# Kernel tuning notes

Measured on AMD Instinct MI355X. Metric: run time of the kernel, lower is better.

## Reference

```python
import jax, jax.numpy as jnp
import numpy as np


def setup_inputs() -> dict:
    key = jax.random.key(0)
    k1, k2, k3, k4 = jax.random.split(key, 4)
    T, H, E, I = 4096, 1024, 8, 3584
    return {
        "hidden_states": jax.random.normal(k1, (T, H), dtype=jnp.float32),
        "gate_w": jax.random.normal(k2, (H, E), dtype=jnp.float32) * 0.02,
        "w1": jax.random.normal(k3, (E, H, I), dtype=jnp.float32) * 0.02,
        "w2": jax.random.normal(k4, (E, I, H), dtype=jnp.float32) * 0.02,
        "top_k": 2,
    }


def reference(hidden_states, gate_w, w1, w2, top_k):
    # Router: logits -> softmax -> top-k -> renormalize (Mixtral / vLLM fused_moe)
    router_logits = hidden_states @ gate_w                    # [T, E]
    probs = jax.nn.softmax(router_logits, axis=-1)
    top_vals, top_idx = jax.lax.top_k(probs, top_k)           # [T, K]
    top_vals = top_vals / jnp.sum(top_vals, axis=-1, keepdims=True)
    E = gate_w.shape[1]
    # Dense per-(token, expert) combine weights, zero for non-selected experts
    dense_w = jnp.sum(jax.nn.one_hot(top_idx, E, dtype=hidden_states.dtype)
                      * top_vals[..., None], axis=1)          # [T, E]
    # Expert MLP: silu(x @ w1[e]) @ w2[e], weighted by routing probs
    act = jax.nn.silu(jnp.einsum('th,ehi->tei', hidden_states, w1))  # [T, E, I]
    act = act * dense_w[:, :, None]
    out = jnp.einsum('tei,eih->th', act, w2)                  # [T, H]
    return out
```

## Files before the change

### kernel.cpp

```cpp
#include <hip/hip_runtime.h>
#include <hip/hip_bf16.h>

#define T_TOK 4096
#define H_DIM 1024
#define E_NUM 8
#define I_DIM 3584
#define NPAIR (T_TOK * 2)
#define MAX_RT 72

#define BM 128
#define BN 128
#define BK 64

typedef __attribute__((ext_vector_type(8))) short bf16x8;
typedef __attribute__((ext_vector_type(4))) float f32x4;
typedef __attribute__((ext_vector_type(8))) unsigned short ushort8_t;
typedef __attribute__((ext_vector_type(4))) unsigned short ushort4_t;

__device__ __forceinline__ unsigned short f2bf(float x) {
  unsigned int u = __float_as_uint(x);
  unsigned int r = (u + 0x7FFFu + ((u >> 16) & 1u)) >> 16;
  return (unsigned short)r;
}

__device__ __forceinline__ void gload16(const void* g, unsigned short* l) {
  __builtin_amdgcn_global_load_lds(
      (const __attribute__((address_space(1))) void*)g,
      (__attribute__((address_space(3))) void*)l, 16, 0, 0);
}

__global__ void transpose_cvt(const float* __restrict__ src,
                              unsigned short* __restrict__ dst, int R, int C) {
  __shared__ float tile[64][65];
  const int e = blockIdx.z;
  const int c0 = blockIdx.x * 64, r0 = blockIdx.y * 64;
  const float* s = src + (size_t)e * R * C;
  unsigned short* d = dst + (size_t)e * R * C;
  const int th = threadIdx.x;
  const int tr = th >> 4;
  const int tc4 = (th & 15) * 4;
#pragma unroll
  for (int it = 0; it < 4; ++it) {
    const int r = it * 16 + tr;
    float4 v = *reinterpret_cast<const float4*>(s + (size_t)(r0 + r) * C + c0 + tc4);
    tile[r][tc4] = v.x; tile[r][tc4 + 1] = v.y; tile[r][tc4 + 2] = v.z; tile[r][tc4 + 3] = v.w;
  }
  __syncthreads();
  const int wc = th >> 3;
  const int wr = (th & 7) * 8;
#pragma unroll
  for (int it = 0; it < 2; ++it) {
    const int c = it * 32 + wc;
    ushort8_t o;
#pragma unroll
    for (int j = 0; j < 8; ++j) o[j] = f2bf(tile[wr + j][c]);
    *reinterpret_cast<ushort8_t*>(d + (size_t)(c0 + c) * R + r0 + wr) = o;
  }
}

__global__ void router_kernel(const float* __restrict__ hs, const float* __restrict__ gw,
                              unsigned short* __restrict__ hsb,
                              int* __restrict__ eid, float* __restrict__ wgt,
                              int* __restrict__ counts) {
  __shared__ float s_gw[8192];
  __shared__ int s_cnt[E_NUM];
  const int th = threadIdx.x;
  for (int u = th; u < 2048; u += 256) {
    const f32x4 v = *reinterpret_cast<const f32x4*>(gw + u * 4);
    *reinterpret_cast<f32x4*>(&s_gw[(u ^ ((u >> 3) & 7)) * 4]) = v;
  }
  if (th < E_NUM) s_cnt[th] = 0;
  __syncthreads();

  const int l = th & 63, w = th >> 6;
#pragma unroll 1
  for (int tt = 0; tt < 4; ++tt) {
    const int t = blockIdx.x * 16 + w * 4 + tt;
    const float* hrow = hs + (size_t)t * H_DIM;
    unsigned short* brow = hsb + (size_t)t * H_DIM;
    float acc[E_NUM];
#pragma unroll
    for (int e = 0; e < E_NUM; ++e) acc[e] = 0.f;
#pragma unroll
    for (int i = 0; i < 4; ++i) {
      const int h0 = i * 256 + l * 4;
      const f32x4 x = *reinterpret_cast<const f32x4*>(hrow + h0);
      ushort4_t o = { f2bf(x[0]), f2bf(x[1]), f2bf(x[2]), f2bf(x[3]) };
      *reinterpret_cast<ushort4_t*>(brow + h0) = o;
#pragma unroll
      for (int j = 0; j < 4; ++j) {
        const int h = h0 + j;
        const int p0 = (h * 2) ^ ((h >> 2) & 7);
        const f32x4 g0 = *reinterpret_cast<const f32x4*>(&s_gw[p0 * 4]);
        const f32x4 g1 = *reinterpret_cast<const f32x4*>(&s_gw[(p0 ^ 1) * 4]);
        acc[0] += x[j] * g0[0]; acc[1] += x[j] * g0[1];
        acc[2] += x[j] * g0[2]; acc[3] += x[j] * g0[3];
        acc[4] += x[j] * g1[0]; acc[5] += x[j] * g1[1];
        acc[6] += x[j] * g1[2]; acc[7] += x[j] * g1[3];
      }
    }
#pragma unroll
    for (int e = 0; e < E_NUM; ++e) {
#pragma unroll
      for (int off = 1; off < 64; off <<= 1) acc[e] += __shfl_xor(acc[e], off);
    }
    if (l == 0) {
      int i1 = 0;
#pragma unroll
      for (int e = 1; e < E_NUM; ++e) if (acc[e] > acc[i1]) i1 = e;
      int i2 = (i1 == 0) ? 1 : 0;
#pragma unroll
      for (int e = 0; e < E_NUM; ++e) if (e != i1 && acc[e] > acc[i2]) i2 = e;
      const float e2 = __expf(acc[i2] - acc[i1]);
      const float inv = 1.f / (1.f + e2);
      eid[t * 2] = i1;     wgt[t * 2] = inv;
      eid[t * 2 + 1] = i2; wgt[t * 2 + 1] = e2 * inv;
      atomicAdd(&s_cnt[i1], 1);
      atomicAdd(&s_cnt[i2], 1);
    }
  }
  __syncthreads();
  if (th < E_NUM && s_cnt[th] > 0) atomicAdd(&counts[th], s_cnt[th]);
}

__global__ void scatter_kernel(const int* __restrict__ eid, const int* __restrict__ counts,
                               int* __restrict__ fill, int* __restrict__ rowmap,
                               int* __restrict__ posmap) {
  __shared__ int hist[E_NUM], base[E_NUM];
  const int th = threadIdx.x;
  const int p = blockIdx.x * 256 + th;
  if (th < E_NUM) hist[th] = 0;
  __syncthreads();
  const int e = eid[p];
  const int rloc = atomicAdd(&hist[e], 1);
  __syncthreads();
  if (th < E_NUM) base[th] = (hist[th] > 0) ? atomicAdd(&fill[th], hist[th]) : 0;
  __syncthreads();
  int off = 0;
#pragma unroll
  for (int i = 0; i < E_NUM; ++i) off += (i < e) ? counts[i] : 0;
  const int pos = off + base[e] + rloc;
  rowmap[pos] = p;
  posmap[p] = pos;
}

__global__ void combine_kernel(const float* __restrict__ res, const int* __restrict__ posmap,
                               float* __restrict__ out) {
  const int t = blockIdx.x;
  const int th = threadIdx.x;
  const int a = posmap[t * 2];
  const int b = posmap[t * 2 + 1];
  const float4 va = *reinterpret_cast<const float4*>(res + (size_t)a * H_DIM + th * 4);
  const float4 vb = *reinterpret_cast<const float4*>(res + (size_t)b * H_DIM + th * 4);
  float4 o = { va.x + vb.x, va.y + vb.y, va.z + vb.z, va.w + vb.w };
  *reinterpret_cast<float4*>(out + (size_t)t * H_DIM + th * 4) = o;
}

template <int MODE, int NCT>
__launch_bounds__(256, 4)
__global__ void moe_gemm(const unsigned short* __restrict__ hsb,
                         const unsigned short* __restrict__ wt,
                         const unsigned short* __restrict__ act_in,
                         unsigned short* __restrict__ act_out,
                         float* __restrict__ res,
                         const int* __restrict__ counts,
                         const int* __restrict__ rowmap,
                         const float* __restrict__ wgt) {
  constexpr int KD = (MODE == 0) ? H_DIM : I_DIM;
  constexpr int NWG = MAX_RT * NCT;

  __shared__ unsigned short As[BM * BK];
  __shared__ unsigned short Bs[BN * BK];
  __shared__ float s_w[BM];

  const int bid = blockIdx.x;
  const int wgid = (bid & 7) * (NWG / 8) + (bid >> 3);
  const int rt = wgid / NCT;
  const int ct = wgid % NCT;

  int e = -1, loc_rt = 0, off_e = 0, cnt = 0;
  {
    int acc_t = 0, off = 0;
#pragma unroll
    for (int ee = 0; ee < E_NUM; ++ee) {
      const int c = counts[ee];
      const int nt = (c + BM - 1) >> 7;
      if (e < 0 && rt < acc_t + nt) { e = ee; loc_rt = rt - acc_t; off_e = off; cnt = c; }
      acc_t += nt; off += c;
    }
  }
  if (e < 0) return;

  const int cnt_local = min(BM, cnt - loc_rt * BM);
  const int r_base = off_e + loc_rt * BM;
  const int th = threadIdx.x;
  const int lane = th & 63, wid = th >> 6;

  if (MODE == 1 && th < BM) {
    int r = loc_rt * BM + th;
    if (r >= cnt) r = cnt - 1;
    s_w[th] = wgt[rowmap[off_e + r]];
  }

  const int n0 = ct * BN;
  const unsigned short* wbase = wt + (size_t)e * ((size_t)I_DIM * H_DIM) + (size_t)n0 * KD;

  const int srow = lane >> 3;
  const int cg = (lane & 7) ^ srow;
  const char* aptr[4];
  const char* bptr[4];
#pragma unroll
  for (int i = 0; i < 4; ++i) {
    const int r = i * 32 + wid * 8 + srow;
    const int rr = (r < cnt_local) ? r : (cnt_local - 1);
    if (MODE == 0) {
      const int tok = rowmap[off_e + loc_rt * BM + rr] >> 1;
      aptr[i] = (const char*)(hsb + (size_t)tok * H_DIM) + cg * 16;
    } else {
      aptr[i] = (const char*)(act_in + (size_t)(r_base + rr) * I_DIM) + cg * 16;
    }
    bptr[i] = (const char*)(wbase + (size_t)r * KD) + cg * 16;
  }
  unsigned short* dstA[4];
  unsigned short* dstB[4];
#pragma unroll
  for (int i = 0; i < 4; ++i) {
    dstA[i] = &As[(i * 32 + wid * 8) * BK];
    dstB[i] = &Bs[(i * 32 + wid * 8) * BK];
  }

  f32x4 acc[4][4];
#pragma unroll
  for (int m = 0; m < 4; ++m)
#pragma unroll
    for (int n = 0; n < 4; ++n) acc[m][n] = (f32x4){0.f, 0.f, 0.f, 0.f};

  const int wm = (wid >> 1) * 64;
  const int wn = (wid & 1) * 64;
  const int fr = lane & 15;
  const int fq = lane >> 4;
  const int sxor = fr & 7;

  for (int k0 = 0; k0 < KD; k0 += BK) {
    const int kb = k0 * 2;
#pragma unroll
    for (int i = 0; i < 4; ++i) gload16(aptr[i] + kb, dstA[i]);
#pragma unroll
    for (int i = 0; i < 4; ++i) gload16(bptr[i] + kb, dstB[i]);
    __syncthreads();

#pragma unroll
    for (int kk = 0; kk < 2; ++kk) {
      bf16x8 af[4], bf[4];
#pragma unroll
      for (int m = 0; m < 4; ++m)
        af[m] = *reinterpret_cast<const bf16x8*>(
            &As[(wm + m * 16 + fr) * BK + ((kk * 4 + fq) ^ sxor) * 8]);
#pragma unroll
      for (int n = 0; n < 4; ++n)
        bf[n] = *reinterpret_cast<const bf16x8*>(
            &Bs[(wn + n * 16 + fr) * BK + ((kk * 4 + fq) ^ sxor) * 8]);
#pragma unroll
      for (int m = 0; m < 4; ++m)
#pragma unroll
        for (int n = 0; n < 4; ++n)
          acc[m][n] = __builtin_amdgcn_mfma_f32_16x16x32_bf16(af[m], bf[n], acc[m][n], 0, 0, 0);
    }
    __syncthreads();
  }

#pragma unroll
  for (int m = 0; m < 4; ++m) {
    const int row = wm + m * 16 + fq * 4;
#pragma unroll
    for (int n = 0; n < 4; ++n) {
      const int col = wn + n * 16 + fr;
#pragma unroll
      for (int r = 0; r < 4; ++r) {
        const int rw = row + r;
        if (rw < cnt_local) {
          const float x = acc[m][n][r];
          if (MODE == 0) {
            const float s = x / (1.f + __expf(-x));
            act_out[(size_t)(r_base + rw) * I_DIM + n0 + col] = f2bf(s);
          } else {
            res[(size_t)(r_base + rw) * H_DIM + n0 + col] = x * s_w[rw];
          }
        }
      }
    }
  }
}

extern "C" void kernel_launch(void* const* d_in, const int* in_sizes, int n_in,
                              void* d_out, int out_size, void* d_ws, size_t ws_size,
                              hipStream_t stream) {
  const float* hs = (const float*)d_in[0];
  const float* gw = (const float*)d_in[1];
  const float* w1 = (const float*)d_in[2];
  const float* w2 = (const float*)d_in[3];
  float* out = (float*)d_out;

  char* ws = (char*)d_ws;
  const size_t WMAT = (size_t)E_NUM * I_DIM * H_DIM * 2;
  unsigned short* w1t = (unsigned short*)ws;
  unsigned short* w2t = (unsigned short*)(ws + WMAT);
  unsigned short* act = (unsigned short*)(ws + 2 * WMAT);
  unsigned short* hsb = (unsigned short*)(ws + 3 * WMAT);
  float* res = (float*)w1t;
  char* small = ws + 3 * WMAT + (size_t)T_TOK * H_DIM * 2;
  int* eid = (int*)small;
  float* wgt = (float*)(small + NPAIR * 4);
  int* rowmap = (int*)(small + 2 * NPAIR * 4);
  int* posmap = (int*)(small + 3 * NPAIR * 4);
  int* counts = (int*)(small + 4 * NPAIR * 4);
  int* fill = counts + 8;

  hipMemsetAsync(counts, 0, 16 * sizeof(int), stream);

  transpose_cvt<<<dim3(I_DIM / 64, H_DIM / 64, E_NUM), 256, 0, stream>>>(w1, w1t, H_DIM, I_DIM);
  transpose_cvt<<<dim3(H_DIM / 64, I_DIM / 64, E_NUM), 256, 0, stream>>>(w2, w2t, I_DIM, H_DIM);

  router_kernel<<<T_TOK / 16, 256, 0, stream>>>(hs, gw, hsb, eid, wgt, counts);
  scatter_kernel<<<NPAIR / 256, 256, 0, stream>>>(eid, counts, fill, rowmap, posmap);

  moe_gemm<0, I_DIM / BN><<<MAX_RT * (I_DIM / BN), 256, 0, stream>>>(
      hsb, w1t, nullptr, act, nullptr, counts, rowmap, wgt);
  moe_gemm<1, H_DIM / BN><<<MAX_RT * (H_DIM / BN), 256, 0, stream>>>(
      hsb, w2t, act, nullptr, res, counts, rowmap, wgt);

  combine_kernel<<<T_TOK, 256, 0, stream>>>(res, posmap, out);
}
```

Baseline: 286.3 us.

## Fuse weight transposes and router into one prep kernel; narrow second GEMM tile

Merges the two weight transpose-convert launches and the router launch into a single prep kernel that picks its role by block index and shares one shared-memory buffer. This removes two launches and lets the router work overlap with the tail of the transposes. The down-projection GEMM drops to a 64-wide N tile with a 4x1 warp layout and an occupancy hint of 5. That doubles its workgroup count, giving better CU fill on the small N dimension, at the cost of less reuse of the A tile.

```diff
diff --git a/kernel.cpp b/kernel.cpp
--- a/kernel.cpp
+++ b/kernel.cpp
@@ -9,7 +9,6 @@
 #define MAX_RT 72
 
 #define BM 128
-#define BN 128
 #define BK 64
 
 typedef __attribute__((ext_vector_type(8))) short bf16x8;
@@ -29,11 +28,11 @@
       (__attribute__((address_space(3))) void*)l, 16, 0, 0);
 }
 
-__global__ void transpose_cvt(const float* __restrict__ src,
-                              unsigned short* __restrict__ dst, int R, int C) {
-  __shared__ float tile[64][65];
-  const int e = blockIdx.z;
-  const int c0 = blockIdx.x * 64, r0 = blockIdx.y * 64;
+__device__ __forceinline__ void transpose_body(const float* __restrict__ src,
+                                               unsigned short* __restrict__ dst,
+                                               int R, int C, int e, int c0, int r0,
+                                               char* smem) {
+  float (*tile)[65] = reinterpret_cast<float (*)[65]>(smem);
   const float* s = src + (size_t)e * R * C;
   unsigned short* d = dst + (size_t)e * R * C;
   const int th = threadIdx.x;
@@ -58,12 +57,13 @@
   }
 }
 
-__global__ void router_kernel(const float* __restrict__ hs, const float* __restrict__ gw,
-                              unsigned short* __restrict__ hsb,
-                              int* __restrict__ eid, float* __restrict__ wgt,
-                              int* __restrict__ counts) {
-  __shared__ float s_gw[8192];
-  __shared__ int s_cnt[E_NUM];
+__device__ __forceinline__ void router_body(const float* __restrict__ hs,
+                                            const float* __restrict__ gw,
+                                            unsigned short* __restrict__ hsb,
+                                            int* __restrict__ eid, float* __restrict__ wgt,
+                                            int* __restrict__ counts, int rbid, char* smem) {
+  float* s_gw = reinterpret_cast<float*>(smem);
+  int* s_cnt = reinterpret_cast<int*>(smem + 32768);
   const int th = threadIdx.x;
   for (int u = th; u < 2048; u += 256) {
     const f32x4 v = *reinterpret_cast<const f32x4*>(gw + u * 4);
@@ -75,7 +75,7 @@
   const int l = th & 63, w = th >> 6;
 #pragma unroll 1
   for (int tt = 0; tt < 4; ++tt) {
-    const int t = blockIdx.x * 16 + w * 4 + tt;
+    const int t = rbid * 16 + w * 4 + tt;
     const float* hrow = hs + (size_t)t * H_DIM;
     unsigned short* brow = hsb + (size_t)t * H_DIM;
     float acc[E_NUM];
@@ -123,6 +123,26 @@
   if (th < E_NUM && s_cnt[th] > 0) atomicAdd(&counts[th], s_cnt[th]);
 }
 
+__global__ __launch_bounds__(256) void prep_kernel(
+    const float* __restrict__ w1, const float* __restrict__ w2,
+    const float* __restrict__ hs, const float* __restrict__ gw,
+    unsigned short* __restrict__ w1t, unsigned short* __restrict__ w2t,
+    unsigned short* __restrict__ hsb,
+    int* __restrict__ eid, float* __restrict__ wgt, int* __restrict__ counts) {
+  __shared__ char smem[33024];
+  const int bid = blockIdx.x;
+  if (bid < 7168) {
+    const int e = bid / 896, rem = bid % 896;
+    transpose_body(w1, w1t, H_DIM, I_DIM, e, (rem % 56) * 64, (rem / 56) * 64, smem);
+  } else if (bid < 14336) {
+    const int idx = bid - 7168;
+    const int e = idx / 896, rem = idx % 896;
+    transpose_body(w2, w2t, I_DIM, H_DIM, e, (rem % 16) * 64, (rem / 16) * 64, smem);
+  } else {
+    router_body(hs, gw, hsb, eid, wgt, counts, bid - 14336, smem);
+  }
+}
+
 __global__ void scatter_kernel(const int* __restrict__ eid, const int* __restrict__ counts,
                                int* __restrict__ fill, int* __restrict__ rowmap,
                                int* __restrict__ posmap) {
@@ -156,8 +176,8 @@
   *reinterpret_cast<float4*>(out + (size_t)t * H_DIM + th * 4) = o;
 }
 
-template <int MODE, int NCT>
-__launch_bounds__(256, 4)
+template <int MODE, int NCT, int OCC>
+__launch_bounds__(256, OCC)
 __global__ void moe_gemm(const unsigned short* __restrict__ hsb,
                          const unsigned short* __restrict__ wt,
                          const unsigned short* __restrict__ act_in,
@@ -167,10 +187,13 @@
                          const int* __restrict__ rowmap,
                          const float* __restrict__ wgt) {
   constexpr int KD = (MODE == 0) ? H_DIM : I_DIM;
+  constexpr int BN_ = (MODE == 0) ? 128 : 64;
+  constexpr int MFR = (MODE == 0) ? 4 : 2;
+  constexpr int NBR = BN_ / 32;
   constexpr int NWG = MAX_RT * NCT;
 
   __shared__ unsigned short As[BM * BK];
-  __shared__ unsigned short Bs[BN * BK];
+  __shared__ unsigned short Bs[BN_ * BK];
   __shared__ float s_w[BM];
 
   const int bid = blockIdx.x;
@@ -202,13 +225,13 @@
     s_w[th] = wgt[rowmap[off_e + r]];
   }
 
-  const int n0 = ct * BN;
+  const int n0 = ct * BN_;
   const unsigned short* wbase = wt + (size_t)e * ((size_t)I_DIM * H_DIM) + (size_t)n0 * KD;
 
   const int srow = lane >> 3;
   const int cg = (lane & 7) ^ srow;
   const char* aptr[4];
-  const char* bptr[4];
+  const char* bptr[NBR];
 #pragma unroll
   for (int i = 0; i < 4; ++i) {
     const int r = i * 32 + wid * 8 + srow;
@@ -219,24 +242,27 @@
     } else {
       aptr[i] = (const char*)(act_in + (size_t)(r_base + rr) * I_DIM) + cg * 16;
     }
-    bptr[i] = (const char*)(wbase + (size_t)r * KD) + cg * 16;
+  }
+#pragma unroll
+  for (int j = 0; j < NBR; ++j) {
+    const int r = j * 32 + wid * 8 + srow;
+    bptr[j] = (const char*)(wbase + (size_t)r * KD) + cg * 16;
   }
   unsigned short* dstA[4];
-  unsigned short* dstB[4];
-#pragma unroll
-  for (int i = 0; i < 4; ++i) {
-    dstA[i] = &As[(i * 32 + wid * 8) * BK];
-    dstB[i] = &Bs[(i * 32 + wid * 8) * BK];
-  }
-
-  f32x4 acc[4][4];
-#pragma unroll
-  for (int m = 0; m < 4; ++m)
+  unsigned short* dstB[NBR];
+#pragma unroll
+  for (int i = 0; i < 4; ++i) dstA[i] = &As[(i * 32 + wid * 8) * BK];
+#pragma unroll
+  for (int j = 0; j < NBR; ++j) dstB[j] = &Bs[(j * 32 + wid * 8) * BK];
+
+  f32x4 acc[MFR][4];
+#pragma unroll
+  for (int m = 0; m < MFR; ++m)
 #pragma unroll
     for (int n = 0; n < 4; ++n) acc[m][n] = (f32x4){0.f, 0.f, 0.f, 0.f};
 
-  const int wm = (wid >> 1) * 64;
-  const int wn = (wid & 1) * 64;
+  const int wm = (MODE == 0) ? (wid >> 1) * 64 : wid * 32;
+  const int wn = (MODE == 0) ? (wid & 1) * 64 : 0;
   const int fr = lane & 15;
   const int fq = lane >> 4;
   const int sxor = fr & 7;
@@ -246,14 +272,14 @@
 #pragma unroll
     for (int i = 0; i < 4; ++i) gload16(aptr[i] + kb, dstA[i]);
 #pragma unroll
-    for (int i = 0; i < 4; ++i) gload16(bptr[i] + kb, dstB[i]);
+    for (int j = 0; j < NBR; ++j) gload16(bptr[j] + kb, dstB[j]);
     __syncthreads();
 
 #pragma unroll
     for (int kk = 0; kk < 2; ++kk) {
-      bf16x8 af[4], bf[4];
-#pragma unroll
-      for (int m = 0; m < 4; ++m)
+      bf16x8 af[MFR], bf[4];
+#pragma unroll
+      for (int m = 0; m < MFR; ++m)
         af[m] = *reinterpret_cast<const bf16x8*>(
             &As[(wm + m * 16 + fr) * BK + ((kk * 4 + fq) ^ sxor) * 8]);
 #pragma unroll
@@ -261,7 +287,7 @@
         bf[n] = *reinterpret_cast<const bf16x8*>(
             &Bs[(wn + n * 16 + fr) * BK + ((kk * 4 + fq) ^ sxor) * 8]);
 #pragma unroll
-      for (int m = 0; m < 4; ++m)
+      for (int m = 0; m < MFR; ++m)
 #pragma unroll
         for (int n = 0; n < 4; ++n)
           acc[m][n] = __builtin_amdgcn_mfma_f32_16x16x32_bf16(af[m], bf[n], acc[m][n], 0, 0, 0);
@@ -270,7 +296,7 @@
   }
 
 #pragma unroll
-  for (int m = 0; m < 4; ++m) {
+  for (int m = 0; m < MFR; ++m) {
     const int row = wm + m * 16 + fq * 4;
 #pragma unroll
     for (int n = 0; n < 4; ++n) {
@@ -318,15 +344,12 @@
 
   hipMemsetAsync(counts, 0, 16 * sizeof(int), stream);
 
-  transpose_cvt<<<dim3(I_DIM / 64, H_DIM / 64, E_NUM), 256, 0, stream>>>(w1, w1t, H_DIM, I_DIM);
-  transpose_cvt<<<dim3(H_DIM / 64, I_DIM / 64, E_NUM), 256, 0, stream>>>(w2, w2t, I_DIM, H_DIM);
-
-  router_kernel<<<T_TOK / 16, 256, 0, stream>>>(hs, gw, hsb, eid, wgt, counts);
+  prep_kernel<<<14592, 256, 0, stream>>>(w1, w2, hs, gw, w1t, w2t, hsb, eid, wgt, counts);
   scatter_kernel<<<NPAIR / 256, 256, 0, stream>>>(eid, counts, fill, rowmap, posmap);
 
-  moe_gemm<0, I_DIM / BN><<<MAX_RT * (I_DIM / BN), 256, 0, stream>>>(
+  moe_gemm<0, I_DIM / 128, 4><<<MAX_RT * (I_DIM / 128), 256, 0, stream>>>(
       hsb, w1t, nullptr, act, nullptr, counts, rowmap, wgt);
-  moe_gemm<1, H_DIM / BN><<<MAX_RT * (H_DIM / BN), 256, 0, stream>>>(
+  moe_gemm<1, H_DIM / 64, 5><<<MAX_RT * (H_DIM / 64), 256, 0, stream>>>(
       hsb, w2t, act, nullptr, res, counts, rowmap, wgt);
 
   combine_kernel<<<T_TOK, 256, 0, stream>>>(res, posmap, out);
```

Result: faster. 261.1 us (-8.8%).

## Shrink GEMM N-tile to 64, raise occupancy, and merge weight transposes into one launch

Applied to the files above, without the earlier changes.

Halves the GEMM tile width (BN 128→64), reorganizing the four waves as a 4x1 stack of 32-row slices that each hold half as many accumulators. The minimum-blocks hint in launch bounds goes from 4 to 5 for more occupancy and twice as many workgroups. The two weight transpose-convert launches are merged into one launch with a flat block index. The trade-off is lower arithmetic intensity per tile, so A tiles are reloaded twice as often.

```diff
diff --git a/kernel.cpp b/kernel.cpp
--- a/kernel.cpp
+++ b/kernel.cpp
@@ -9,7 +9,7 @@
 #define MAX_RT 72
 
 #define BM 128
-#define BN 128
+#define BN 64
 #define BK 64
 
 typedef __attribute__((ext_vector_type(8))) short bf16x8;
@@ -29,11 +29,25 @@
       (__attribute__((address_space(3))) void*)l, 16, 0, 0);
 }
 
-__global__ void transpose_cvt(const float* __restrict__ src,
-                              unsigned short* __restrict__ dst, int R, int C) {
+__global__ __launch_bounds__(256) void wt_transpose(
+    const float* __restrict__ w1, const float* __restrict__ w2,
+    unsigned short* __restrict__ w1t, unsigned short* __restrict__ w2t) {
   __shared__ float tile[64][65];
-  const int e = blockIdx.z;
-  const int c0 = blockIdx.x * 64, r0 = blockIdx.y * 64;
+  const int bid = blockIdx.x;
+  const float* src;
+  unsigned short* dst;
+  int R, C, e, c0, r0;
+  if (bid < 7168) {
+    const int rem = bid % 896;
+    e = bid / 896; R = H_DIM; C = I_DIM;
+    c0 = (rem % 56) * 64; r0 = (rem / 56) * 64;
+    src = w1; dst = w1t;
+  } else {
+    const int idx = bid - 7168, rem = idx % 896;
+    e = idx / 896; R = I_DIM; C = H_DIM;
+    c0 = (rem % 16) * 64; r0 = (rem / 16) * 64;
+    src = w2; dst = w2t;
+  }
   const float* s = src + (size_t)e * R * C;
   unsigned short* d = dst + (size_t)e * R * C;
   const int th = threadIdx.x;
@@ -157,7 +171,7 @@
 }
 
 template <int MODE, int NCT>
-__launch_bounds__(256, 4)
+__launch_bounds__(256, 5)
 __global__ void moe_gemm(const unsigned short* __restrict__ hsb,
                          const unsigned short* __restrict__ wt,
                          const unsigned short* __restrict__ act_in,
@@ -208,7 +222,7 @@
   const int srow = lane >> 3;
   const int cg = (lane & 7) ^ srow;
   const char* aptr[4];
-  const char* bptr[4];
+  const char* bptr[2];
 #pragma unroll
   for (int i = 0; i < 4; ++i) {
     const int r = i * 32 + wid * 8 + srow;
@@ -219,24 +233,26 @@
     } else {
       aptr[i] = (const char*)(act_in + (size_t)(r_base + rr) * I_DIM) + cg * 16;
     }
-    bptr[i] = (const char*)(wbase + (size_t)r * KD) + cg * 16;
+  }
+#pragma unroll
+  for (int j = 0; j < 2; ++j) {
+    const int r = j * 32 + wid * 8 + srow;
+    bptr[j] = (const char*)(wbase + (size_t)r * KD) + cg * 16;
   }
   unsigned short* dstA[4];
-  unsigned short* dstB[4];
-#pragma unroll
-  for (int i = 0; i < 4; ++i) {
-    dstA[i] = &As[(i * 32 + wid * 8) * BK];
-    dstB[i] = &Bs[(i * 32 + wid * 8) * BK];
-  }
-
-  f32x4 acc[4][4];
-#pragma unroll
-  for (int m = 0; m < 4; ++m)
+  unsigned short* dstB[2];
+#pragma unroll
+  for (int i = 0; i < 4; ++i) dstA[i] = &As[(i * 32 + wid * 8) * BK];
+#pragma unroll
+  for (int j = 0; j < 2; ++j) dstB[j] = &Bs[(j * 32 + wid * 8) * BK];
+
+  f32x4 acc[2][4];
+#pragma unroll
+  for (int m = 0; m < 2; ++m)
 #pragma unroll
     for (int n = 0; n < 4; ++n) acc[m][n] = (f32x4){0.f, 0.f, 0.f, 0.f};
 
-  const int wm = (wid >> 1) * 64;
-  const int wn = (wid & 1) * 64;
+  const int wm = wid * 32;
   const int fr = lane & 15;
   const int fq = lane >> 4;
   const int sxor = fr & 7;
@@ -246,22 +262,22 @@
 #pragma unroll
     for (int i = 0; i < 4; ++i) gload16(aptr[i] + kb, dstA[i]);
 #pragma unroll
-    for (int i = 0; i < 4; ++i) gload16(bptr[i] + kb, dstB[i]);
+    for (int j = 0; j < 2; ++j) gload16(bptr[j] + kb, dstB[j]);
     __syncthreads();
 
 #pragma unroll
     for (int kk = 0; kk < 2; ++kk) {
-      bf16x8 af[4], bf[4];
-#pragma unroll
-      for (int m = 0; m < 4; ++m)
+      bf16x8 af[2], bf[4];
+#pragma unroll
+      for (int m = 0; m < 2; ++m)
         af[m] = *reinterpret_cast<const bf16x8*>(
             &As[(wm + m * 16 + fr) * BK + ((kk * 4 + fq) ^ sxor) * 8]);
 #pragma unroll
       for (int n = 0; n < 4; ++n)
         bf[n] = *reinterpret_cast<const bf16x8*>(
-            &Bs[(wn + n * 16 + fr) * BK + ((kk * 4 + fq) ^ sxor) * 8]);
-#pragma unroll
-      for (int m = 0; m < 4; ++m)
+            &Bs[(n * 16 + fr) * BK + ((kk * 4 + fq) ^ sxor) * 8]);
+#pragma unroll
+      for (int m = 0; m < 2; ++m)
 #pragma unroll
         for (int n = 0; n < 4; ++n)
           acc[m][n] = __builtin_amdgcn_mfma_f32_16x16x32_bf16(af[m], bf[n], acc[m][n], 0, 0, 0);
@@ -270,11 +286,11 @@
   }
 
 #pragma unroll
-  for (int m = 0; m < 4; ++m) {
+  for (int m = 0; m < 2; ++m) {
     const int row = wm + m * 16 + fq * 4;
 #pragma unroll
     for (int n = 0; n < 4; ++n) {
-      const int col = wn + n * 16 + fr;
+      const int col = n0 + n * 16 + fr;
 #pragma unroll
       for (int r = 0; r < 4; ++r) {
         const int rw = row + r;
@@ -282,9 +298,9 @@
           const float x = acc[m][n][r];
           if (MODE == 0) {
             const float s = x / (1.f + __expf(-x));
-            act_out[(size_t)(r_base + rw) * I_DIM + n0 + col] = f2bf(s);
+            act_out[(size_t)(r_base + rw) * I_DIM + col] = f2bf(s);
           } else {
-            res[(size_t)(r_base + rw) * H_DIM + n0 + col] = x * s_w[rw];
+            res[(size_t)(r_base + rw) * H_DIM + col] = x * s_w[rw];
           }
         }
       }
@@ -318,9 +334,7 @@
 
   hipMemsetAsync(counts, 0, 16 * sizeof(int), stream);
 
-  transpose_cvt<<<dim3(I_DIM / 64, H_DIM / 64, E_NUM), 256, 0, stream>>>(w1, w1t, H_DIM, I_DIM);
-  transpose_cvt<<<dim3(H_DIM / 64, I_DIM / 64, E_NUM), 256, 0, stream>>>(w2, w2t, I_DIM, H_DIM);
-
+  wt_transpose<<<14336, 256, 0, stream>>>(w1, w2, w1t, w2t);
   router_kernel<<<T_TOK / 16, 256, 0, stream>>>(hs, gw, hsb, eid, wgt, counts);
   scatter_kernel<<<NPAIR / 256, 256, 0, stream>>>(eid, counts, fill, rowmap, posmap);
 
```

After: 312.5 us. 1.09x slower.
